# Performance work log

Measured on AMD Instinct MI355X. Metric: run time of the kernel, lower is better.

## Reference

```python
import jax, jax.numpy as jnp
import numpy as np

D = 768
NH = 12
HD = D // NH
N_MLP = 3072
LN_EPS = 1e-6


def layer_norm(x, g, b, eps=LN_EPS):
    mu = jnp.mean(x, axis=-1, keepdims=True)
    var = jnp.mean(jnp.square(x - mu), axis=-1, keepdims=True)
    return (x - mu) * jax.lax.rsqrt(var + eps) * g + b


def setup_inputs() -> dict:
    key = jax.random.key(0)
    ks = jax.random.split(key, 6)
    x = jax.random.normal(ks[0], (2, 4096, D), dtype=jnp.float32)
    # torch Linear weights are (out, in); init std=0.02, zero bias
    W_qkv = 0.02 * jax.random.normal(ks[1], (3 * D, D), dtype=jnp.float32)
    b_qkv = jnp.zeros((3 * D,), dtype=jnp.float32)
    W_proj = 0.02 * jax.random.normal(ks[2], (D, D), dtype=jnp.float32)
    b_proj = jnp.zeros((D,), dtype=jnp.float32)
    W1 = 0.02 * jax.random.normal(ks[3], (N_MLP, D), dtype=jnp.float32)
    b1 = jnp.zeros((N_MLP,), dtype=jnp.float32)
    W2 = 0.02 * jax.random.normal(ks[4], (D, N_MLP), dtype=jnp.float32)
    b2 = jnp.zeros((D,), dtype=jnp.float32)
    g1 = jnp.ones((D,), dtype=jnp.float32)
    beta1 = jnp.zeros((D,), dtype=jnp.float32)
    g2 = jnp.ones((D,), dtype=jnp.float32)
    beta2 = jnp.zeros((D,), dtype=jnp.float32)
    return dict(x=x, W_qkv=W_qkv, b_qkv=b_qkv, W_proj=W_proj, b_proj=b_proj,
                W1=W1, b1=b1, W2=W2, b2=b2,
                g1=g1, beta1=beta1, g2=g2, beta2=beta2)


def reference(x, W_qkv, b_qkv, W_proj, b_proj, W1, b1, W2, b2, g1, beta1, g2, beta2):
    B, T, d = x.shape
    scale = HD ** (-0.5)
    # --- attention branch (pre-norm) ---
    h = layer_norm(x, g1, beta1)
    qkv = h @ W_qkv.T + b_qkv                      # [B,T,3d]
    qkv = qkv.reshape(B, T, 3, NH, HD)
    q, k, v = qkv[:, :, 0], qkv[:, :, 1], qkv[:, :, 2]  # [B,T,NH,HD]
    logits = jnp.einsum('bthc,bshc->bhts', q, k) * scale
    attn = jax.nn.softmax(logits, axis=-1)
    out = jnp.einsum('bhts,bshc->bthc', attn, v).reshape(B, T, d)
    out = out @ W_proj.T + b_proj
    x = x + out
    # --- MLP branch (pre-norm) ---
    h = layer_norm(x, g2, beta2)
    h = jax.nn.gelu(h @ W1.T + b1, approximate=False)
    h = h @ W2.T + b2
    return x + h
```

## Files before the change

kernel.cpp:

```cpp
#include <hip/hip_runtime.h>
#include <cmath>

typedef __attribute__((ext_vector_type(4))) float f32x4;
typedef __attribute__((ext_vector_type(16))) float f32x16;
typedef __attribute__((ext_vector_type(8))) __bf16 bf16x8;
typedef __attribute__((ext_vector_type(8))) unsigned short u16x8;
typedef __attribute__((ext_vector_type(4))) unsigned short u16x4;
typedef __attribute__((ext_vector_type(2))) unsigned int u32x2;
typedef __attribute__((ext_vector_type(4))) unsigned int u32x4;

#define DEV __device__ __forceinline__

DEV unsigned short f2b(float v) {
  __bf16 b = (__bf16)v;
  return __builtin_bit_cast(unsigned short, b);
}

DEV unsigned int cvtpk(float lo, float hi) {
  unsigned int r;
  asm("v_cvt_pk_bf16_f32 %0, %1, %2" : "=v"(r) : "v"(lo), "v"(hi));
  return r;
}

DEV float exp2a(float x) {
  float r;
  asm("v_exp_f32 %0, %1" : "=v"(r) : "v"(x));
  return r;
}

DEV void swap32(unsigned int& x, unsigned int& y) {
  asm("v_permlane32_swap_b32 %0, %1" : "+v"(x), "+v"(y));
}

DEV u32x2 tr_b16(const unsigned short* p) {
  u32x2 r;
  asm volatile("ds_read_b64_tr_b16 %0, %1"
               : "=v"(r)
               : "v"((unsigned int)(unsigned long long)p)
               : "memory");
  return r;
}

DEV void gll16(const void* g, const void* l) {
  __builtin_amdgcn_global_load_lds(
      (const __attribute__((address_space(1))) unsigned int*)(unsigned long long)g,
      (__attribute__((address_space(3))) unsigned int*)(unsigned int)(unsigned long long)l,
      16, 0, 0);
}

DEV float bflo(unsigned int u) { return __builtin_bit_cast(float, u << 16); }
DEV float bfhi(unsigned int u) { return __builtin_bit_cast(float, u & 0xFFFF0000u); }

DEV void ln_row(const float* __restrict__ xr, const float* __restrict__ g,
                const float* __restrict__ be, unsigned short* __restrict__ orow, int l) {
  float4 v[3];
  float s = 0.f, sq = 0.f;
#pragma unroll
  for (int j = 0; j < 3; ++j) {
    v[j] = ((const float4*)xr)[l + 64 * j];
    s += v[j].x + v[j].y + v[j].z + v[j].w;
    sq += v[j].x * v[j].x + v[j].y * v[j].y + v[j].z * v[j].z + v[j].w * v[j].w;
  }
#pragma unroll
  for (int m = 1; m < 64; m <<= 1) {
    s += __shfl_xor(s, m);
    sq += __shfl_xor(sq, m);
  }
  float mu = s * (1.f / 768.f);
  float var = sq * (1.f / 768.f) - mu * mu;
  float rs = rsqrtf(var + 1e-6f);
#pragma unroll
  for (int j = 0; j < 3; ++j) {
    int c4 = l + 64 * j;
    float4 gv = ((const float4*)g)[c4];
    float4 bv = ((const float4*)be)[c4];
    u16x4 o = {f2b((v[j].x - mu) * rs * gv.x + bv.x),
               f2b((v[j].y - mu) * rs * gv.y + bv.y),
               f2b((v[j].z - mu) * rs * gv.z + bv.z),
               f2b((v[j].w - mu) * rs * gv.w + bv.w)};
    *(u16x4*)(orow + c4 * 4) = o;
  }
}

__global__ void k_ln(const float* __restrict__ x, const float* __restrict__ g,
                     const float* __restrict__ be, unsigned short* __restrict__ out) {
  int row = blockIdx.x * 4 + (threadIdx.x >> 6);
  int l = threadIdx.x & 63;
  ln_row(x + (size_t)row * 768, g, be, out + (size_t)row * 768, l);
}

__global__ void k_pre(const float* __restrict__ x, const float* __restrict__ g,
                      const float* __restrict__ be, unsigned short* __restrict__ h1,
                      const float* __restrict__ s0, const float* __restrict__ s1,
                      const float* __restrict__ s2, const float* __restrict__ s3,
                      unsigned short* __restrict__ wdst) {
  int bid = blockIdx.x;
  if (bid < 2048) {
    int row = bid * 4 + (threadIdx.x >> 6);
    int l = threadIdx.x & 63;
    ln_row(x + (size_t)row * 768, g, be, h1 + (size_t)row * 768, l);
    return;
  }
  int i = (bid - 2048) * 256 + threadIdx.x;
  const float* s;
  unsigned short* d;
  if (i < 442368) {
    s = s0 + (size_t)i * 4;
    d = wdst + (size_t)i * 4;
  } else if (i < 589824) {
    int j = i - 442368;
    s = s1 + (size_t)j * 4;
    d = wdst + 1769472 + (size_t)j * 4;
  } else if (i < 1179648) {
    int j = i - 589824;
    s = s2 + (size_t)j * 4;
    d = wdst + 2359296 + (size_t)j * 4;
  } else {
    int j = i - 1179648;
    s = s3 + (size_t)j * 4;
    d = wdst + 4718592 + (size_t)j * 4;
  }
  float4 v = *(const float4*)s;
  u16x4 o = {f2b(v.x), f2b(v.y), f2b(v.z), f2b(v.w)};
  *(u16x4*)d = o;
}

template <int MODE, int BM, int BN>
__global__ __launch_bounds__(256, 2) void k_gemm(
    const unsigned short* __restrict__ A, const unsigned short* __restrict__ Bw,
    const float* __restrict__ bias, const float* __restrict__ res,
    void* __restrict__ outp, int N, int K) {
  __shared__ unsigned short As[2][BM * 64];
  __shared__ unsigned short Bs[2][BN * 64];
  constexpr int MR = BM / 32;
  constexpr int NR = BN / 32;
  constexpr int AI = BM / 32;
  constexpr int BI = BN / 32;
  constexpr int LPT = AI + BI;
  const int tid = threadIdx.x;
  const int w = tid >> 6, l = tid & 63;
  const int wr = w >> 1, wc = w & 1;
  const int lr = l & 15, lg = l >> 4;
  const int nwg = gridDim.x * gridDim.y;
  const int bid = blockIdx.y * gridDim.x + blockIdx.x;
  const int swz = (bid & 7) * (nwg >> 3) + (bid >> 3);
  const int bx = swz % gridDim.x, by = swz / gridDim.x;
  const int brow = by * BM, bcol = bx * BN;

  auto stage = [&](int buf, int kt) {
#pragma unroll
    for (int i = 0; i < AI; ++i) {
      int c = i * 256 + tid;
      int row = c >> 3, cg = (c & 7) ^ (row & 7);
      gll16(A + (size_t)(brow + row) * K + kt + cg * 8,
            (const char*)&As[buf][0] + (i * 256 + (w << 6)) * 16);
    }
#pragma unroll
    for (int i = 0; i < BI; ++i) {
      int c = i * 256 + tid;
      int row = c >> 3, cg = (c & 7) ^ (row & 7);
      gll16(Bw + (size_t)(bcol + row) * K + kt + cg * 8,
            (const char*)&Bs[buf][0] + (i * 256 + (w << 6)) * 16);
    }
  };

  stage(0, 0);
  if (64 < K) stage(1, 64);
  f32x4 acc[MR][NR] = {};
  for (int kt = 0, t = 0; kt < K; kt += 64, ++t) {
    const int cur = t & 1;
    if (kt + 64 < K) {
      if constexpr (LPT == 8)
        asm volatile("s_waitcnt vmcnt(8)" ::: "memory");
      else if constexpr (LPT == 6)
        asm volatile("s_waitcnt vmcnt(6)" ::: "memory");
      else
        asm volatile("s_waitcnt vmcnt(4)" ::: "memory");
    } else {
      asm volatile("s_waitcnt vmcnt(0)" ::: "memory");
    }
    __builtin_amdgcn_s_barrier();
    __builtin_amdgcn_sched_barrier(0);
    bf16x8 af[MR][2], bfr[NR][2];
#pragma unroll
    for (int m = 0; m < MR; ++m) {
      int row = wr * (BM / 2) + m * 16 + lr;
#pragma unroll
      for (int s = 0; s < 2; ++s)
        af[m][s] = *(const bf16x8*)&As[cur][row * 64 + (((s * 4 + lg) ^ (row & 7)) << 3)];
    }
#pragma unroll
    for (int n = 0; n < NR; ++n) {
      int row = wc * (BN / 2) + n * 16 + lr;
#pragma unroll
      for (int s = 0; s < 2; ++s)
        bfr[n][s] = *(const bf16x8*)&Bs[cur][row * 64 + (((s * 4 + lg) ^ (row & 7)) << 3)];
    }
    asm volatile("s_waitcnt lgkmcnt(0)" ::: "memory");
    __builtin_amdgcn_sched_barrier(0);
    __builtin_amdgcn_s_barrier();
    if (kt + 128 < K) stage(cur, kt + 128);
    __builtin_amdgcn_s_setprio(1);
#pragma unroll
    for (int s = 0; s < 2; ++s)
#pragma unroll
      for (int m = 0; m < MR; ++m)
#pragma unroll
        for (int n = 0; n < NR; ++n)
          acc[m][n] =
              __builtin_amdgcn_mfma_f32_16x16x32_bf16(af[m][s], bfr[n][s], acc[m][n], 0, 0, 0);
    __builtin_amdgcn_s_setprio(0);
  }
#pragma unroll
  for (int n = 0; n < NR; ++n) {
    int col = bcol + wc * (BN / 2) + n * 16 + lr;
    float bv = bias[col];
#pragma unroll
    for (int m = 0; m < MR; ++m) {
      int row0 = brow + wr * (BM / 2) + m * 16 + lg * 4;
#pragma unroll
      for (int r = 0; r < 4; ++r) {
        size_t idx = (size_t)(row0 + r) * N + col;
        float v = acc[m][n][r] + bv;
        if (MODE == 0) {
          ((unsigned short*)outp)[idx] = f2b(v);
        } else if (MODE == 1) {
          ((float*)outp)[idx] = v + res[idx];
        } else if (MODE == 2) {
          ((unsigned short*)outp)[idx] = f2b(0.5f * v * (1.f + erff(v * 0.70710678f)));
        } else {
          ((float*)outp)[idx] = v + res[idx];
        }
      }
    }
  }
}

__global__ __launch_bounds__(256, 4) void k_attn(const unsigned short* __restrict__ qkv,
                                                 u32x4* __restrict__ Opk,
                                                 float* __restrict__ ml) {
  __shared__ unsigned short Ks[2][64 * 64];
  __shared__ unsigned short Vs[2][4 * 64 * 16];
  const int tid = threadIdx.x;
  const int w = tid >> 6, l = tid & 63;
  const int lq = l & 31, hi = l >> 5;
  const int p = blockIdx.x;
  const int linear = (p & 7) * 192 + (p >> 3);
  const int bh = linear >> 6, rem = linear & 63;
  const int qt = rem >> 1, half = rem & 1;
  const int b = bh / 12, h = bh % 12;
  const size_t base = (size_t)b * 4096 * 2304;
  const int qbase = qt * 128 + w * 32;
  const int kv0 = half * 2048;

  const float SC = 0.18033688f;
  bf16x8 qb[4];
#pragma unroll
  for (int s = 0; s < 4; ++s) {
    u16x8 raw = *(const u16x8*)(qkv + base + (size_t)(qbase + lq) * 2304 + h * 64 +
                                s * 16 + hi * 8);
    u32x4 pk;
#pragma unroll
    for (int d = 0; d < 4; ++d) {
      float f0 = __builtin_bit_cast(float, (unsigned int)raw[2 * d] << 16) * SC;
      float f1 = __builtin_bit_cast(float, (unsigned int)raw[2 * d + 1] << 16) * SC;
      pk[d] = cvtpk(f0, f1);
    }
    qb[s] = __builtin_bit_cast(bf16x8, pk);
  }

  const unsigned short* pK = qkv + base + (size_t)(kv0 + 16 * w + (l >> 3)) * 2304 + 768 +
                             h * 64 + (((l & 7) ^ ((l >> 3) & 7)) << 3);
  const unsigned short* pV = qkv + base + (size_t)(kv0 + (l >> 1)) * 2304 + 1536 + h * 64 +
                             w * 16 + ((l & 1) << 3);
  const size_t STEP = (size_t)64 * 2304;

  {
    const char* dK = (const char*)&Ks[0][0] + w * 2048;
    const char* dV = (const char*)&Vs[0][0] + w * 2048;
    gll16(pK, dK);
    gll16(pK + 8 * 2304, dK + 1024);
    gll16(pV, dV);
    gll16(pV + 32 * 2304, dV + 1024);
    pK += STEP;
    pV += STEP;
  }

  f32x16 O[2] = {};
  float lrun = 0.f;

  int it = 0;
  for (int t = 0; t < 32; ++t, it ^= 1) {
    asm volatile("s_waitcnt vmcnt(0)" ::: "memory");
    __syncthreads();
    if (t < 31) {
      const char* dK = (const char*)&Ks[it ^ 1][0] + w * 2048;
      const char* dV = (const char*)&Vs[it ^ 1][0] + w * 2048;
      gll16(pK, dK);
      gll16(pK + 8 * 2304, dK + 1024);
      gll16(pV, dV);
      gll16(pV + 32 * 2304, dV + 1024);
      pK += STEP;
      pV += STEP;
    }

    f32x16 st[2] = {{0}, {0}};
    __builtin_amdgcn_s_setprio(1);
#pragma unroll
    for (int kt = 0; kt < 2; ++kt) {
      int key = kt * 32 + lq;
#pragma unroll
      for (int s = 0; s < 4; ++s) {
        bf16x8 ka =
            *(const bf16x8*)&Ks[it][key * 64 + ((s * 16 + hi * 8) ^ ((key & 7) << 3))];
        st[kt] = __builtin_amdgcn_mfma_f32_32x32x16_bf16(ka, qb[s], st[kt], 0, 0, 0);
      }
    }
    __builtin_amdgcn_s_setprio(0);

    float s0 = 0.f, s1 = 0.f, s2 = 0.f, s3 = 0.f;
#pragma unroll
    for (int kt = 0; kt < 2; ++kt) {
#pragma unroll
      for (int r = 0; r < 16; r += 4) {
        float p0 = exp2a(st[kt][r + 0]);
        float p1 = exp2a(st[kt][r + 1]);
        float p2 = exp2a(st[kt][r + 2]);
        float p3 = exp2a(st[kt][r + 3]);
        st[kt][r + 0] = p0;
        st[kt][r + 1] = p1;
        st[kt][r + 2] = p2;
        st[kt][r + 3] = p3;
        s0 += p0;
        s1 += p1;
        s2 += p2;
        s3 += p3;
      }
    }
    float ssum = (s0 + s1) + (s2 + s3);
    lrun += ssum + __shfl_xor(ssum, 32);

    u32x4 pf[4];
#pragma unroll
    for (int kt = 0; kt < 2; ++kt)
#pragma unroll
      for (int h2 = 0; h2 < 2; ++h2) {
        int r0 = h2 * 8;
        unsigned int a0 = cvtpk(st[kt][r0 + 0], st[kt][r0 + 1]);
        unsigned int a1 = cvtpk(st[kt][r0 + 2], st[kt][r0 + 3]);
        unsigned int b0 = cvtpk(st[kt][r0 + 4], st[kt][r0 + 5]);
        unsigned int b1 = cvtpk(st[kt][r0 + 6], st[kt][r0 + 7]);
        swap32(a0, b0);
        swap32(a1, b1);
        pf[kt * 2 + h2] = u32x4{a0, a1, b0, b1};
      }

#pragma unroll
    for (int hb = 0; hb < 2; ++hb) {
      u32x2 vt[4][2];
      const unsigned short* vbase = &Vs[it][(hb * 2 + (lq >> 4)) * 1024 + (lq & 15)];
#pragma unroll
      for (int s = 0; s < 4; ++s)
#pragma unroll
        for (int t2 = 0; t2 < 2; ++t2)
          vt[s][t2] = tr_b16(vbase + ((s * 16 + hi * 8 + t2 * 4) << 4));
      asm volatile("s_waitcnt lgkmcnt(0)" ::: "memory");
      __builtin_amdgcn_sched_barrier(0);
      __builtin_amdgcn_s_setprio(1);
#pragma unroll
      for (int s = 0; s < 4; ++s) {
        u32x4 vv = {vt[s][0].x, vt[s][0].y, vt[s][1].x, vt[s][1].y};
        O[hb] = __builtin_amdgcn_mfma_f32_32x32x16_bf16(
            __builtin_bit_cast(bf16x8, vv), __builtin_bit_cast(bf16x8, pf[s]), O[hb], 0, 0, 0);
      }
      __builtin_amdgcn_s_setprio(0);
    }
  }

  if (hi == 0) ml[(linear * 4 + w) * 32 + lq] = lrun;
#pragma unroll
  for (int hb = 0; hb < 2; ++hb)
#pragma unroll
    for (int v = 0; v < 2; ++v) {
      u32x4 pkv = {cvtpk(O[hb][8 * v + 0], O[hb][8 * v + 1]),
                   cvtpk(O[hb][8 * v + 2], O[hb][8 * v + 3]),
                   cvtpk(O[hb][8 * v + 4], O[hb][8 * v + 5]),
                   cvtpk(O[hb][8 * v + 6], O[hb][8 * v + 7])};
      Opk[((linear * 4 + w) * 4 + hb * 2 + v) * 64 + l] = pkv;
    }
}

__global__ __launch_bounds__(256) void k_merge(const u32x4* __restrict__ Opk,
                                               const float* __restrict__ ml,
                                               unsigned short* __restrict__ out) {
  const int g = blockIdx.x;
  const int bh = g >> 5, qt = g & 31;
  const int b = bh / 12, h = bh % 12;
  const int tid = threadIdx.x;
  const int w = tid >> 6, l = tid & 63;
  const int lq = l & 31, hi = l >> 5;
  const int bidA = bh * 64 + qt * 2;
  const int bidB = bidA + 1;
  float l0 = ml[(bidA * 4 + w) * 32 + lq];
  float l1 = ml[(bidB * 4 + w) * 32 + lq];
  float rl = 1.f / (l0 + l1);
  const int t = qt * 128 + w * 32 + lq;
  unsigned short* orow = out + (size_t)(b * 4096 + t) * 768 + h * 64;
#pragma unroll
  for (int hb = 0; hb < 2; ++hb)
#pragma unroll
    for (int v = 0; v < 2; ++v) {
      u32x4 va = Opk[((bidA * 4 + w) * 4 + hb * 2 + v) * 64 + l];
      u32x4 vb = Opk[((bidB * 4 + w) * 4 + hb * 2 + v) * 64 + l];
      unsigned int dw[4];
#pragma unroll
      for (int d = 0; d < 4; ++d) {
        float lo = (bflo(va[d]) + bflo(vb[d])) * rl;
        float hi2 = (bfhi(va[d]) + bfhi(vb[d])) * rl;
        dw[d] = cvtpk(lo, hi2);
      }
      *(u32x2*)(orow + hb * 32 + 8 * (2 * v) + 4 * hi) = u32x2{dw[0], dw[1]};
      *(u32x2*)(orow + hb * 32 + 8 * (2 * v + 1) + 4 * hi) = u32x2{dw[2], dw[3]};
    }
}

extern "C" void kernel_launch(void* const* d_in, const int* in_sizes, int n_in,
                              void* d_out, int out_size, void* d_ws, size_t ws_size,
                              hipStream_t stream) {
  const float* x = (const float*)d_in[0];
  const float* Wqkv = (const float*)d_in[1];
  const float* bqkv = (const float*)d_in[2];
  const float* Wproj = (const float*)d_in[3];
  const float* bproj = (const float*)d_in[4];
  const float* W1 = (const float*)d_in[5];
  const float* b1 = (const float*)d_in[6];
  const float* W2 = (const float*)d_in[7];
  const float* b2 = (const float*)d_in[8];
  const float* g1 = (const float*)d_in[9];
  const float* be1 = (const float*)d_in[10];
  const float* g2 = (const float*)d_in[11];
  const float* be2 = (const float*)d_in[12];

  char* ws = (char*)d_ws;
  unsigned short* wqkv = (unsigned short*)(ws + 0);
  unsigned short* wproj = (unsigned short*)(ws + 3538944);
  unsigned short* ww1 = (unsigned short*)(ws + 4718592);
  unsigned short* ww2 = (unsigned short*)(ws + 9437184);
  unsigned short* h1 = (unsigned short*)(ws + 14155776);
  unsigned short* qkvb = (unsigned short*)(ws + 26738688);
  unsigned short* attno = (unsigned short*)(ws + 64487424);
  float* x1 = (float*)(ws + 77070336);
  unsigned short* h2 = (unsigned short*)(ws + 102236160);
  unsigned short* m1 = (unsigned short*)(ws + 114819072);
  u32x4* Opk = (u32x4*)m1;
  float* mlbuf = (float*)h1;

  k_pre<<<8960, 256, 0, stream>>>(x, g1, be1, h1, Wqkv, Wproj, W1, W2, wqkv);

  k_gemm<0, 128, 128><<<dim3(18, 64), 256, 0, stream>>>(h1, wqkv, bqkv, nullptr, qkvb, 2304, 768);
  k_attn<<<1536, 256, 0, stream>>>(qkvb, Opk, mlbuf);
  k_merge<<<768, 256, 0, stream>>>(Opk, mlbuf, attno);
  k_gemm<1, 128, 64><<<dim3(12, 64), 256, 0, stream>>>(attno, wproj, bproj, x, x1, 768, 768);
  k_ln<<<2048, 256, 0, stream>>>(x1, g2, be2, h2);
  k_gemm<2, 128, 128><<<dim3(24, 64), 256, 0, stream>>>(h2, ww1, b1, nullptr, m1, 3072, 768);
  k_gemm<3, 128, 64><<<dim3(12, 64), 256, 0, stream>>>(m1, ww2, b2, x1, (float*)d_out, 768, 3072);
}
```

Measured before the change: 334.4 us.

## Triple-buffer K/V tiles and software-pipeline QK^T of next tile with PV

The attention kernel moves from two to three LDS buffers for K/V and restructures the main loop so the QK^T MFMAs for tile t+1 are issued while the softmax and PV MFMAs of tile t proceed. Async global-to-LDS loads are issued two tiles ahead. The aim is to hide exp/softmax latency and the load wait behind matrix work. In exchange, LDS use rises by half, which may limit occupancy under the 4-blocks launch bound, and more registers stay live because the V fragments for both halves are held at once.

```diff
diff --git a/kernel.cpp b/kernel.cpp
--- a/kernel.cpp
+++ b/kernel.cpp
@@ -239,8 +239,8 @@
 __global__ __launch_bounds__(256, 4) void k_attn(const unsigned short* __restrict__ qkv,
                                                  u32x4* __restrict__ Opk,
                                                  float* __restrict__ ml) {
-  __shared__ unsigned short Ks[2][64 * 64];
-  __shared__ unsigned short Vs[2][4 * 64 * 16];
+  __shared__ unsigned short Ks[3][64 * 64];
+  __shared__ unsigned short Vs[3][4 * 64 * 16];
   const int tid = threadIdx.x;
   const int w = tid >> 6, l = tid & 63;
   const int lq = l & 31, hi = l >> 5;
@@ -275,49 +275,45 @@
                              w * 16 + ((l & 1) << 3);
   const size_t STEP = (size_t)64 * 2304;
 
-  {
-    const char* dK = (const char*)&Ks[0][0] + w * 2048;
-    const char* dV = (const char*)&Vs[0][0] + w * 2048;
+  auto stage = [&](int buf) {
+    const char* dK = (const char*)&Ks[buf][0] + w * 2048;
+    const char* dV = (const char*)&Vs[buf][0] + w * 2048;
     gll16(pK, dK);
     gll16(pK + 8 * 2304, dK + 1024);
     gll16(pV, dV);
     gll16(pV + 32 * 2304, dV + 1024);
     pK += STEP;
     pV += STEP;
-  }
+  };
+
+  f32x16 st[2];
+  auto qkc = [&](int kb) {
+    f32x16 z = {};
+    st[0] = z;
+    st[1] = z;
+#pragma unroll
+    for (int kt = 0; kt < 2; ++kt) {
+      int key = kt * 32 + lq;
+#pragma unroll
+      for (int s = 0; s < 4; ++s) {
+        bf16x8 ka =
+            *(const bf16x8*)&Ks[kb][key * 64 + ((s * 16 + hi * 8) ^ ((key & 7) << 3))];
+        st[kt] = __builtin_amdgcn_mfma_f32_32x32x16_bf16(ka, qb[s], st[kt], 0, 0, 0);
+      }
+    }
+  };
+
+  stage(0);
+  stage(1);
+  asm volatile("s_waitcnt vmcnt(4)" ::: "memory");
+  __builtin_amdgcn_s_barrier();
+  qkc(0);
 
   f32x16 O[2] = {};
   float lrun = 0.f;
-
-  int it = 0;
-  for (int t = 0; t < 32; ++t, it ^= 1) {
-    asm volatile("s_waitcnt vmcnt(0)" ::: "memory");
-    __syncthreads();
-    if (t < 31) {
-      const char* dK = (const char*)&Ks[it ^ 1][0] + w * 2048;
-      const char* dV = (const char*)&Vs[it ^ 1][0] + w * 2048;
-      gll16(pK, dK);
-      gll16(pK + 8 * 2304, dK + 1024);
-      gll16(pV, dV);
-      gll16(pV + 32 * 2304, dV + 1024);
-      pK += STEP;
-      pV += STEP;
-    }
-
-    f32x16 st[2] = {{0}, {0}};
-    __builtin_amdgcn_s_setprio(1);
-#pragma unroll
-    for (int kt = 0; kt < 2; ++kt) {
-      int key = kt * 32 + lq;
-#pragma unroll
-      for (int s = 0; s < 4; ++s) {
-        bf16x8 ka =
-            *(const bf16x8*)&Ks[it][key * 64 + ((s * 16 + hi * 8) ^ ((key & 7) << 3))];
-        st[kt] = __builtin_amdgcn_mfma_f32_32x32x16_bf16(ka, qb[s], st[kt], 0, 0, 0);
-      }
-    }
-    __builtin_amdgcn_s_setprio(0);
-
+  int cur = 0, nxt = 1, stg = 2;
+
+  for (int t = 0; t < 32; ++t) {
     float s0 = 0.f, s1 = 0.f, s2 = 0.f, s3 = 0.f;
 #pragma unroll
     for (int kt = 0; kt < 2; ++kt) {
@@ -355,26 +351,52 @@
         pf[kt * 2 + h2] = u32x4{a0, a1, b0, b1};
       }
 
-#pragma unroll
-    for (int hb = 0; hb < 2; ++hb) {
-      u32x2 vt[4][2];
-      const unsigned short* vbase = &Vs[it][(hb * 2 + (lq >> 4)) * 1024 + (lq & 15)];
-#pragma unroll
-      for (int s = 0; s < 4; ++s)
-#pragma unroll
-        for (int t2 = 0; t2 < 2; ++t2)
-          vt[s][t2] = tr_b16(vbase + ((s * 16 + hi * 8 + t2 * 4) << 4));
-      asm volatile("s_waitcnt lgkmcnt(0)" ::: "memory");
-      __builtin_amdgcn_sched_barrier(0);
+    u32x2 vt[2][4][2];
+    if (t < 31) {
+      asm volatile("s_waitcnt vmcnt(0)" ::: "memory");
+      __syncthreads();
+      if (t < 30) stage(stg);
+#pragma unroll
+      for (int hb = 0; hb < 2; ++hb) {
+        const unsigned short* vbase = &Vs[cur][(hb * 2 + (lq >> 4)) * 1024 + (lq & 15)];
+#pragma unroll
+        for (int s = 0; s < 4; ++s)
+#pragma unroll
+          for (int t2 = 0; t2 < 2; ++t2)
+            vt[hb][s][t2] = tr_b16(vbase + ((s * 16 + hi * 8 + t2 * 4) << 4));
+      }
       __builtin_amdgcn_s_setprio(1);
+      qkc(nxt);
+      __builtin_amdgcn_s_setprio(0);
+    } else {
+#pragma unroll
+      for (int hb = 0; hb < 2; ++hb) {
+        const unsigned short* vbase = &Vs[cur][(hb * 2 + (lq >> 4)) * 1024 + (lq & 15)];
+#pragma unroll
+        for (int s = 0; s < 4; ++s)
+#pragma unroll
+          for (int t2 = 0; t2 < 2; ++t2)
+            vt[hb][s][t2] = tr_b16(vbase + ((s * 16 + hi * 8 + t2 * 4) << 4));
+      }
+    }
+
+    asm volatile("s_waitcnt lgkmcnt(0)" ::: "memory");
+    __builtin_amdgcn_sched_barrier(0);
+    __builtin_amdgcn_s_setprio(1);
+#pragma unroll
+    for (int hb = 0; hb < 2; ++hb)
 #pragma unroll
       for (int s = 0; s < 4; ++s) {
-        u32x4 vv = {vt[s][0].x, vt[s][0].y, vt[s][1].x, vt[s][1].y};
+        u32x4 vv = {vt[hb][s][0].x, vt[hb][s][0].y, vt[hb][s][1].x, vt[hb][s][1].y};
         O[hb] = __builtin_amdgcn_mfma_f32_32x32x16_bf16(
             __builtin_bit_cast(bf16x8, vv), __builtin_bit_cast(bf16x8, pf[s]), O[hb], 0, 0, 0);
       }
-      __builtin_amdgcn_s_setprio(0);
-    }
+    __builtin_amdgcn_s_setprio(0);
+
+    int old = cur;
+    cur = nxt;
+    nxt = stg;
+    stg = old;
   }
 
   if (hi == 0) ml[(linear * 4 + w) * 32 + lq] = lrun;
```

New measurement: 357.1 us. +6.8%, slower.

## Add 256x256 eight-wave pipelined GEMM for QKV and MLP-up projections

Applied to the files above, without the earlier changes.

Adds a new GEMM kernel with 512 threads and 256x256 output tiles. It uses double-buffered LDS filled by direct global-to-LDS loads, with staggered A/B prefetch interleaved between four MFMA quadrants, explicit barriers and waitcnts, priority boosting and an XCD-aware block swizzle. The QKV and W1 GEMMs switch to this kernel to get more operand reuse per tile and better load/compute overlap. The trade-off is fewer blocks (288 and 384), which risks tail underutilisation on a 256-CU part, plus 128KB of LDS per block, which limits occupancy.

```diff
diff --git a/kernel.cpp b/kernel.cpp
--- a/kernel.cpp
+++ b/kernel.cpp
@@ -50,6 +50,13 @@
 
 DEV float bflo(unsigned int u) { return __builtin_bit_cast(float, u << 16); }
 DEV float bfhi(unsigned int u) { return __builtin_bit_cast(float, u & 0xFFFF0000u); }
+
+#define BARRIER()                     \
+  __builtin_amdgcn_s_barrier();       \
+  __builtin_amdgcn_sched_barrier(0)
+#define LGKM_FENCE()                                     \
+  asm volatile("s_waitcnt lgkmcnt(0)" ::: "memory");     \
+  __builtin_amdgcn_sched_barrier(0)
 
 DEV void ln_row(const float* __restrict__ xr, const float* __restrict__ g,
                 const float* __restrict__ be, unsigned short* __restrict__ orow, int l) {
@@ -123,6 +130,129 @@
   float4 v = *(const float4*)s;
   u16x4 o = {f2b(v.x), f2b(v.y), f2b(v.z), f2b(v.w)};
   *(u16x4*)d = o;
+}
+
+template <int MODE>
+__global__ __launch_bounds__(512, 2) void k_gemm8p(
+    const unsigned short* __restrict__ A, const unsigned short* __restrict__ Bw,
+    const float* __restrict__ bias, void* __restrict__ outp, int N, int K) {
+  __shared__ unsigned short As[2][256 * 64];
+  __shared__ unsigned short Bs[2][256 * 64];
+  const int tid = threadIdx.x;
+  const int w = tid >> 6, l = tid & 63;
+  const int wm = w >> 2, wn = w & 3;
+  const int lr = l & 15, lg = l >> 4;
+  const int nwg = gridDim.x * gridDim.y;
+  const int bid = blockIdx.y * gridDim.x + blockIdx.x;
+  const int swz = (bid & 7) * (nwg >> 3) + (bid >> 3);
+  const int bx = swz % gridDim.x, by = swz / gridDim.x;
+  const int brow = by * 256, bcol = bx * 256;
+  const int nt = K >> 6;
+
+  auto stA = [&](int s, int kt, int h) {
+#pragma unroll
+    for (int i = 0; i < 2; ++i) {
+      int c = i * 512 + tid;
+      int r = c >> 3, cg = (c & 7) ^ (r & 7);
+      gll16(A + (size_t)(brow + h * 128 + r) * K + kt + cg * 8,
+            (const char*)&As[s][0] + h * 16384 + (i * 512 + (w << 6)) * 16);
+    }
+  };
+  auto stB = [&](int s, int kt, int h) {
+#pragma unroll
+    for (int i = 0; i < 2; ++i) {
+      int c = i * 512 + tid;
+      int r = c >> 3, cg = (c & 7) ^ (r & 7);
+      gll16(Bw + (size_t)(bcol + h * 128 + r) * K + kt + cg * 8,
+            (const char*)&Bs[s][0] + h * 16384 + (i * 512 + (w << 6)) * 16);
+    }
+  };
+
+  f32x4 acc[8][4] = {};
+  bf16x8 af[2][4][2], bf[2][2][2];
+
+#define READ_A(SLOT, MH)                                                       \
+  _Pragma("unroll") for (int m = 0; m < 4; ++m) {                              \
+    int row = wm * 128 + (MH)*64 + m * 16 + lr;                                \
+    _Pragma("unroll") for (int s2 = 0; s2 < 2; ++s2) af[MH][m][s2] =           \
+        *(const bf16x8*)&As[SLOT][row * 64 + (((s2 * 4 + lg) ^ (row & 7)) << 3)]; \
+  }
+#define READ_B(SLOT, NH)                                                       \
+  _Pragma("unroll") for (int n = 0; n < 2; ++n) {                              \
+    int row = wn * 64 + (NH)*32 + n * 16 + lr;                                 \
+    _Pragma("unroll") for (int s2 = 0; s2 < 2; ++s2) bf[NH][n][s2] =           \
+        *(const bf16x8*)&Bs[SLOT][row * 64 + (((s2 * 4 + lg) ^ (row & 7)) << 3)]; \
+  }
+#define MFMA_QUAD(MH, NH)                                                      \
+  __builtin_amdgcn_s_setprio(1);                                               \
+  _Pragma("unroll") for (int s2 = 0; s2 < 2; ++s2)                             \
+  _Pragma("unroll") for (int m = 0; m < 4; ++m)                                \
+  _Pragma("unroll") for (int n = 0; n < 2; ++n) acc[(MH)*4 + m][(NH)*2 + n] =  \
+      __builtin_amdgcn_mfma_f32_16x16x32_bf16(af[MH][m][s2], bf[NH][n][s2],    \
+                                              acc[(MH)*4 + m][(NH)*2 + n], 0, 0, 0); \
+  __builtin_amdgcn_s_setprio(0)
+
+  stA(0, 0, 0);
+  stA(0, 0, 1);
+  stB(0, 0, 0);
+  stB(0, 0, 1);
+  stA(1, 64, 0);
+  stA(1, 64, 1);
+
+  for (int g = 0; g < nt; ++g) {
+    const int slot = g & 1, os = slot ^ 1;
+    const int kt1 = (g + 1) << 6, kt2 = (g + 2) << 6;
+    if (g == nt - 1)
+      asm volatile("s_waitcnt vmcnt(0)" ::: "memory");
+    else
+      asm volatile("s_waitcnt vmcnt(4)" ::: "memory");
+    BARRIER();
+    if (g + 1 < nt) stB(os, kt1, 0);
+    READ_A(slot, 0);
+    READ_B(slot, 0);
+    LGKM_FENCE();
+    MFMA_QUAD(0, 0);
+    BARRIER();
+    if (g + 1 < nt) stB(os, kt1, 1);
+    READ_A(slot, 1);
+    LGKM_FENCE();
+    MFMA_QUAD(1, 0);
+    BARRIER();
+    if (g + 2 < nt) stA(slot, kt2, 0);
+    READ_B(slot, 1);
+    LGKM_FENCE();
+    MFMA_QUAD(0, 1);
+    BARRIER();
+    if (g + 2 < nt) stA(slot, kt2, 1);
+    MFMA_QUAD(1, 1);
+  }
+
+#undef READ_A
+#undef READ_B
+#undef MFMA_QUAD
+
+#pragma unroll
+  for (int nh = 0; nh < 2; ++nh)
+#pragma unroll
+    for (int n = 0; n < 2; ++n) {
+      int col = bcol + wn * 64 + nh * 32 + n * 16 + lr;
+      float bv = bias[col];
+#pragma unroll
+      for (int mh = 0; mh < 2; ++mh)
+#pragma unroll
+        for (int m = 0; m < 4; ++m) {
+          int row0 = brow + wm * 128 + mh * 64 + m * 16 + lg * 4;
+#pragma unroll
+          for (int r = 0; r < 4; ++r) {
+            size_t idx = (size_t)(row0 + r) * N + col;
+            float v = acc[mh * 4 + m][nh * 2 + n][r] + bv;
+            if (MODE == 0)
+              ((unsigned short*)outp)[idx] = f2b(v);
+            else
+              ((unsigned short*)outp)[idx] = f2b(0.5f * v * (1.f + erff(v * 0.70710678f)));
+          }
+        }
+    }
 }
 
 template <int MODE, int BM, int BN>
@@ -457,11 +587,11 @@
 
   k_pre<<<8960, 256, 0, stream>>>(x, g1, be1, h1, Wqkv, Wproj, W1, W2, wqkv);
 
-  k_gemm<0, 128, 128><<<dim3(18, 64), 256, 0, stream>>>(h1, wqkv, bqkv, nullptr, qkvb, 2304, 768);
+  k_gemm8p<0><<<dim3(9, 32), 512, 0, stream>>>(h1, wqkv, bqkv, qkvb, 2304, 768);
   k_attn<<<1536, 256, 0, stream>>>(qkvb, Opk, mlbuf);
   k_merge<<<768, 256, 0, stream>>>(Opk, mlbuf, attno);
   k_gemm<1, 128, 64><<<dim3(12, 64), 256, 0, stream>>>(attno, wproj, bproj, x, x1, 768, 768);
   k_ln<<<2048, 256, 0, stream>>>(x1, g2, be2, h2);
-  k_gemm<2, 128, 128><<<dim3(24, 64), 256, 0, stream>>>(h2, ww1, b1, nullptr, m1, 3072, 768);
+  k_gemm8p<2><<<dim3(12, 32), 512, 0, stream>>>(h2, ww1, b1, m1, 3072, 768);
   k_gemm<3, 128, 64><<<dim3(12, 64), 256, 0, stream>>>(m1, ww2, b2, x1, (float*)d_out, 768, 3072);
 }
```

Result: slower. 345.5 us (+3.3%).
